# Kernel tuning notes

Hardware: AMD Instinct MI355X
Metric: run time of the kernel (lower is better)

Reference implementation:

```python
import jax, jax.numpy as jnp
import numpy as np

EPS = 1e-6      # vector-neuron epsilon
BN_EPS = 1e-5   # torch BatchNorm eps
NEG = 0.2       # LeakyReLU negative slope
K = 20


def knn_idx(flat, k):
    # flat: [B, D, N] flattened (C*3) features; returns kNN indices [B, N, k]
    xx = jnp.sum(flat * flat, axis=1)                     # [B, N]
    inner = jnp.einsum('bdn,bdm->bnm', flat, flat)        # [B, N, N]
    neg_dist = 2.0 * inner - xx[:, :, None] - xx[:, None, :]
    return jax.lax.top_k(neg_dist, k)[1]                  # [B, N, k]


def graph_feature(x, k):
    # x: [B, C, 3, N] -> [B, 2C, 3, N, k] = cat(neighbor - center, center)
    B, C, _, N = x.shape
    idx = knn_idx(x.reshape(B, C * 3, N), k)              # [B, N, k]
    xt = jnp.transpose(x, (0, 3, 1, 2))                   # [B, N, C, 3]
    nbr = jax.vmap(lambda f, i: f[i])(xt, idx)            # [B, N, k, C, 3]
    ctr = jnp.broadcast_to(xt[:, :, None], nbr.shape)
    feat = jnp.concatenate([nbr - ctr, ctr], axis=3)      # [B, N, k, 2C, 3]
    return jnp.transpose(feat, (0, 3, 4, 1, 2))


def vn_bn(x, w, b):
    # VNBatchNorm (training-mode batch stats): normalize the per-vector norm.
    # x: [B, C, 3, ...]
    norm = jnp.sqrt(jnp.sum(x * x, axis=2)) + EPS         # [B, C, ...]
    axes = (0,) + tuple(range(2, norm.ndim))
    mean = jnp.mean(norm, axis=axes, keepdims=True)
    var = jnp.mean((norm - mean) ** 2, axis=axes, keepdims=True)
    shp = (1, -1) + (1,) * (norm.ndim - 2)
    nbn = (norm - mean) / jnp.sqrt(var + BN_EPS) * w.reshape(shp) + b.reshape(shp)
    return x * jnp.expand_dims(nbn / norm, 2)


def vn_lrelu(x, wf, wd, bnw, bnb):
    # VNLinearLeakyReLU: linear over channel dim, VN batchnorm, directional LeakyReLU
    p = jnp.einsum('oi,bi...->bo...', wf, x)
    p = vn_bn(p, bnw, bnb)
    d = jnp.einsum('oi,bi...->bo...', wd, x)
    dot = jnp.sum(p * d, axis=2, keepdims=True)
    dsq = jnp.sum(d * d, axis=2, keepdims=True)
    mask = (dot >= 0).astype(x.dtype)
    return NEG * p + (1.0 - NEG) * (mask * p + (1.0 - mask) * (p - (dot / (dsq + EPS)) * d))


def setup_inputs() -> dict:
    key = jax.random.key(0)
    ks = jax.random.split(key, 12)
    H, C = 64, 128
    lin = lambda k, o, i: jax.random.normal(k, (o, i), jnp.float32) / np.sqrt(i)
    return {
        'x': jax.random.normal(ks[0], (8, 1024, 3), jnp.float32),
        'w1f': lin(ks[1], H, 2), 'w1d': lin(ks[2], H, 2),
        'bn1w': jnp.ones(H), 'bn1b': jnp.zeros(H),
        'w2f': lin(ks[3], H, 2 * H), 'w2d': lin(ks[4], H, 2 * H),
        'bn2w': jnp.ones(H), 'bn2b': jnp.zeros(H),
        'w3f': lin(ks[5], H, 2 * H), 'w3d': lin(ks[6], H, 2 * H),
        'bn3w': jnp.ones(H), 'bn3b': jnp.zeros(H),
        'w4f': lin(ks[7], H, 2 * H), 'w4d': lin(ks[8], H, 2 * H),
        'bn4w': jnp.ones(H), 'bn4b': jnp.zeros(H),
        'wcf': lin(ks[9], C, 4 * H), 'wcd': lin(ks[10], 1, 4 * H),
        'bncw': jnp.ones(C), 'bncb': jnp.zeros(C),
    }


def reference(x, w1f, w1d, bn1w, bn1b, w2f, w2d, bn2w, bn2b,
              w3f, w3d, bn3w, bn3b, w4f, w4d, bn4w, bn4b,
              wcf, wcd, bncw, bncb):
    pts = jnp.transpose(x, (0, 2, 1))[:, None]            # [B, 1, 3, N]
    h = vn_lrelu(graph_feature(pts, K), w1f, w1d, bn1w, bn1b)
    x1 = jnp.mean(h, axis=-1)                             # [B, H, 3, N]
    h = vn_lrelu(graph_feature(x1, K), w2f, w2d, bn2w, bn2b)
    x2 = jnp.mean(h, axis=-1)
    h = vn_lrelu(graph_feature(x2, K), w3f, w3d, bn3w, bn3b)
    x3 = jnp.mean(h, axis=-1)
    h = vn_lrelu(graph_feature(x3, K), w4f, w4d, bn4w, bn4b)
    x4 = jnp.mean(h, axis=-1)
    cat = jnp.concatenate([x1, x2, x3, x4], axis=1)       # [B, 4H, 3, N]
    out = vn_lrelu(cat, wcf, wcd, bncw, bncb)             # [B, c_dim, 3, N]
    return jnp.mean(out, axis=-1)                         # [B, c_dim, 3]
```

## Files before the change

### kernel.cpp

```cpp
#include <hip/hip_runtime.h>

#define NPTS 1024
#define NB 8
#define KNN 20
#define N3 (3*NPTS)
#define CHT 256
#define BSX (CHT*N3)

constexpr int OFF_X0    = 0;
constexpr int OFF_XFEAT = OFF_X0 + NB*N3;
constexpr int OFF_YAP   = OFF_XFEAT + NB*CHT*N3;
constexpr int OFF_YBP   = OFF_YAP + NB*N3*64;
constexpr int OFF_YAD   = OFF_YBP + NB*N3*64;
constexpr int OFF_YBD   = OFF_YAD + NB*N3*64;
constexpr int OFF_XX    = OFF_YBD + NB*N3*64;
constexpr int OFF_WCFT  = OFF_XX + NB*NPTS;
constexpr int OFF_STATS = OFF_WCFT + 256*128;
constexpr int OFF_IDX   = OFF_STATS + 5*256;
constexpr int OFF_PF    = OFF_YAP;
constexpr int OFF_DF    = OFF_YAD;

__global__ void k_transpose(const float* __restrict__ x, float* __restrict__ x0) {
  int t = blockIdx.x*256 + threadIdx.x;
  int b = t >> 10, n = t & 1023;
  const float* p = x + t*3;
  x0[b*N3 + n]          = p[0];
  x0[b*N3 + NPTS + n]   = p[1];
  x0[b*N3 + 2*NPTS + n] = p[2];
}

__global__ void k_xx(const float* __restrict__ Fb, int bs, int D, float* __restrict__ xx) {
  int t = blockIdx.x*256 + threadIdx.x;
  int b = t >> 10, m = t & 1023;
  const float* f = Fb + b*bs + m;
  float a = 0.f;
  for (int d = 0; d < D; ++d) { float v = f[d*NPTS]; a = fmaf(v, v, a); }
  xx[t] = a;
}

__global__ __launch_bounds__(512) void k_knn2(const float* __restrict__ Fb, int bs, int D,
                                              const float* __restrict__ xx,
                                              int* __restrict__ idxo) {
  __shared__ float xs[8][NPTS];
  int g  = blockIdx.x;
  int wg = (g & 7)*64 + (g >> 3);
  int b  = wg >> 6;
  int n0 = (wg & 63) << 4;
  int tid = threadIdx.x;
  int w = tid >> 6, lane = tid & 63;
  const float* f = Fb + b*bs;

  int row0 = n0 + 2*w, row1 = row0 + 1;
  float acc0[16], acc1[16];
  #pragma unroll
  for (int s = 0; s < 16; ++s) { acc0[s] = 0.f; acc1[s] = 0.f; }

  int nt = (D + 7) >> 3;
  for (int t = 0; t < nt; ++t) {
    int d0 = t << 3;
    int cnt = D - d0; if (cnt > 8) cnt = 8;
    __syncthreads();
    #pragma unroll
    for (int u = 0; u < 4; ++u) {
      int e = tid + (u << 9);
      int dd = e >> 8, mq = (e & 255) << 2;
      if (dd < cnt)
        *(float4*)&xs[dd][mq] = *(const float4*)&f[(d0 + dd)*NPTS + mq];
    }
    __syncthreads();
    for (int dd = 0; dd < cnt; ++dd) {
      float rf0 = xs[dd][row0];
      float rf1 = xs[dd][row1];
      #pragma unroll
      for (int s2 = 0; s2 < 4; ++s2) {
        float4 xm = *(const float4*)&xs[dd][(lane << 2) + (s2 << 8)];
        acc0[s2*4+0] = fmaf(rf0, xm.x, acc0[s2*4+0]);
        acc0[s2*4+1] = fmaf(rf0, xm.y, acc0[s2*4+1]);
        acc0[s2*4+2] = fmaf(rf0, xm.z, acc0[s2*4+2]);
        acc0[s2*4+3] = fmaf(rf0, xm.w, acc0[s2*4+3]);
        acc1[s2*4+0] = fmaf(rf1, xm.x, acc1[s2*4+0]);
        acc1[s2*4+1] = fmaf(rf1, xm.y, acc1[s2*4+1]);
        acc1[s2*4+2] = fmaf(rf1, xm.z, acc1[s2*4+2]);
        acc1[s2*4+3] = fmaf(rf1, xm.w, acc1[s2*4+3]);
      }
    }
  }

  float xxm[16];
  #pragma unroll
  for (int s2 = 0; s2 < 4; ++s2) {
    float4 xv = *(const float4*)&xx[b*NPTS + (lane << 2) + (s2 << 8)];
    xxm[s2*4+0] = xv.x; xxm[s2*4+1] = xv.y; xxm[s2*4+2] = xv.z; xxm[s2*4+3] = xv.w;
  }
  float xxr0 = xx[b*NPTS + row0];
  float xxr1 = xx[b*NPTS + row1];
  #pragma unroll
  for (int s = 0; s < 16; ++s) {
    acc0[s] = (2.f*acc0[s] - xxr0) - xxm[s];
    acc1[s] = (2.f*acc1[s] - xxr1) - xxm[s];
  }

  #pragma unroll
  for (int rr = 0; rr < 2; ++rr) {
    int rown = rr ? row1 : row0;
    unsigned taken = 0u;
    int winm = 0;
    for (int it = 0; it < KNN; ++it) {
      float bv = -3.402823466e38f;
      int   bi = 0x7fffffff;
      int   bsl = 0;
      #pragma unroll
      for (int s = 0; s < 16; ++s) {
        int m = (lane << 2) + ((s >> 2) << 8) + (s & 3);
        float v = rr ? acc1[s] : acc0[s];
        bool ok = (((taken >> s) & 1u) == 0u) && (v > bv);
        bv  = ok ? v : bv;
        bi  = ok ? m : bi;
        bsl = ok ? s : bsl;
      }
      int myi = bi, mysl = bsl;
      #pragma unroll
      for (int off = 1; off < 64; off <<= 1) {
        float ov = __shfl_xor(bv, off, 64);
        int   oi = __shfl_xor(bi, off, 64);
        bool tk = (ov > bv) || (ov == bv && oi < bi);
        bv = tk ? ov : bv;
        bi = tk ? oi : bi;
      }
      if (bi == myi) taken |= (1u << (mysl & 15));
      if (lane == it) winm = bi;
    }
    if (lane < KNN) idxo[(b*NPTS + rown)*KNN + lane] = winm;
  }
}

template<int DIN>
__global__ __launch_bounds__(256) void k_linear3(const float* __restrict__ xin, int bsx,
                                                 const float* __restrict__ w,
                                                 float* __restrict__ yA, float* __restrict__ yB) {
  __shared__ float wA[DIN*64], wB[DIN*64];
  int tid = threadIdx.x;
  for (int e = tid; e < 64*DIN; e += 256) {
    int o = e & 63, i = e >> 6;
    float a = w[o*(2*DIN) + i];
    wA[i*64 + o] = a;
    wB[i*64 + o] = w[o*(2*DIN) + DIN + i] - a;
  }
  __syncthreads();
  int o = tid & 63, ns = tid >> 6;
  int b = blockIdx.y / 3, v = blockIdx.y % 3;
  int n0 = blockIdx.x * 64 + ns * 16;
  const float* xb = xin + b*bsx + v*NPTS + n0;
  float ap[16], bp[16];
  #pragma unroll
  for (int j = 0; j < 16; ++j) { ap[j] = 0.f; bp[j] = 0.f; }
  for (int i = 0; i < DIN; ++i) {
    float wa = wA[i*64 + o], wb = wB[i*64 + o];
    #pragma unroll
    for (int q = 0; q < 4; ++q) {
      float4 xv = *(const float4*)&xb[i*N3 + q*4];
      ap[q*4+0] = fmaf(wa, xv.x, ap[q*4+0]); bp[q*4+0] = fmaf(wb, xv.x, bp[q*4+0]);
      ap[q*4+1] = fmaf(wa, xv.y, ap[q*4+1]); bp[q*4+1] = fmaf(wb, xv.y, bp[q*4+1]);
      ap[q*4+2] = fmaf(wa, xv.z, ap[q*4+2]); bp[q*4+2] = fmaf(wb, xv.z, bp[q*4+2]);
      ap[q*4+3] = fmaf(wa, xv.w, ap[q*4+3]); bp[q*4+3] = fmaf(wb, xv.w, bp[q*4+3]);
    }
  }
  int base = ((b*3 + v)*NPTS + n0)*64 + o;
  #pragma unroll
  for (int j = 0; j < 16; ++j) { yA[base + j*64] = ap[j]; yB[base + j*64] = bp[j]; }
}

__global__ __launch_bounds__(256) void k_stats(const float* __restrict__ yAp, const float* __restrict__ yBp,
                                               const int* __restrict__ idxo, float* __restrict__ statsL) {
  __shared__ float rs[256], rss[256];
  int tid = threadIdx.x; int o = tid & 63, w = tid >> 6;
  int blk = blockIdx.x;
  int b = blk >> 6;
  int n0 = (blk & 63) << 4;
  float s = 0.f, ss = 0.f;
  for (int jj = 0; jj < 4; ++jj) {
    int n = n0 + w + (jj << 2);
    int i0 = (b*3*NPTS + n)*64 + o;
    float c0 = yBp[i0], c1 = yBp[i0 + NPTS*64], c2 = yBp[i0 + 2*NPTS*64];
    const int* ir = idxo + (b*NPTS + n)*KNN;
    for (int kk = 0; kk < KNN; ++kk) {
      int m = ir[kk];
      int g = (b*3*NPTS + m)*64 + o;
      float p0 = yAp[g] + c0;
      float p1 = yAp[g + NPTS*64] + c1;
      float p2 = yAp[g + 2*NPTS*64] + c2;
      float nrm = sqrtf(p0*p0 + p1*p1 + p2*p2) + 1e-6f;
      s += nrm; ss = fmaf(nrm, nrm, ss);
    }
  }
  rs[tid] = s; rss[tid] = ss;
  __syncthreads();
  if (tid < 64) {
    float a  = rs[tid]  + rs[tid+64]  + rs[tid+128]  + rs[tid+192];
    float as = rss[tid] + rss[tid+64] + rss[tid+128] + rss[tid+192];
    atomicAdd(&statsL[tid], a);
    atomicAdd(&statsL[128 + tid], as);
  }
}

__global__ __launch_bounds__(256) void k_apply(const float* __restrict__ yAp, const float* __restrict__ yBp,
                                               const float* __restrict__ yAd, const float* __restrict__ yBd,
                                               const int* __restrict__ idxo, const float* __restrict__ statsL,
                                               const float* __restrict__ bnw, const float* __restrict__ bnb,
                                               float* __restrict__ xfeat, int coff) {
  int tid = threadIdx.x; int o = tid & 63, w = tid >> 6;
  int blk = blockIdx.x;
  int b = blk >> 8;
  int n = ((blk & 255) << 2) + w;
  const float cntInv = 1.f / 163840.f;
  float mean = statsL[o] * cntInv;
  float var  = statsL[128 + o] * cntInv - mean*mean;
  float istd = rsqrtf(var + 1e-5f);
  float wN = bnw[o], bN = bnb[o];
  int i0 = (b*3*NPTS + n)*64 + o;
  float cp0 = yBp[i0], cp1 = yBp[i0 + NPTS*64], cp2 = yBp[i0 + 2*NPTS*64];
  float cd0 = yBd[i0], cd1 = yBd[i0 + NPTS*64], cd2 = yBd[i0 + 2*NPTS*64];
  const int* ir = idxo + (b*NPTS + n)*KNN;
  float a0 = 0.f, a1 = 0.f, a2 = 0.f;
  for (int kk = 0; kk < KNN; ++kk) {
    int m = ir[kk];
    int g = (b*3*NPTS + m)*64 + o;
    float p0 = yAp[g] + cp0, p1 = yAp[g + NPTS*64] + cp1, p2 = yAp[g + 2*NPTS*64] + cp2;
    float d0 = yAd[g] + cd0, d1 = yAd[g + NPTS*64] + cd1, d2 = yAd[g + 2*NPTS*64] + cd2;
    float nrm = sqrtf(p0*p0 + p1*p1 + p2*p2) + 1e-6f;
    float sc = ((nrm - mean)*istd*wN + bN) / nrm;
    p0 *= sc; p1 *= sc; p2 *= sc;
    float dot = p0*d0 + p1*d1 + p2*d2;
    float dsq = d0*d0 + d1*d1 + d2*d2;
    float coef = (dot < 0.f) ? (0.8f * dot / (dsq + 1e-6f)) : 0.f;
    a0 += p0 - coef*d0; a1 += p1 - coef*d1; a2 += p2 - coef*d2;
  }
  int ob = ((b*CHT + coff + o)*3)*NPTS + n;
  xfeat[ob]          = a0 * 0.05f;
  xfeat[ob + NPTS]   = a1 * 0.05f;
  xfeat[ob + 2*NPTS] = a2 * 0.05f;
}

__global__ void k_wcfT(const float* __restrict__ wcf, float* __restrict__ wT) {
  int e = blockIdx.x*256 + threadIdx.x;
  int o = e >> 8, i = e & 255;
  wT[i*128 + o] = wcf[e];
}

__global__ __launch_bounds__(256) void k_pF2(const float* __restrict__ xfeat, const float* __restrict__ wT,
                                             float* __restrict__ pF) {
  __shared__ float xs[256][32];
  int tid = threadIdx.x;
  int b = blockIdx.y / 3, v = blockIdx.y % 3;
  int n0 = blockIdx.x * 32;
  const float* xb = xfeat + b*BSX + v*NPTS + n0;
  #pragma unroll
  for (int u = 0; u < 8; ++u) {
    int e = tid + (u << 8);
    int i = e >> 3, sl = (e & 7) << 2;
    *(float4*)&xs[i][sl] = *(const float4*)&xb[i*N3 + sl];
  }
  __syncthreads();
  int o = tid & 127, h = tid >> 7;
  float a[16];
  #pragma unroll
  for (int j = 0; j < 16; ++j) a[j] = 0.f;
  for (int i = 0; i < 256; ++i) {
    float wv = wT[i*128 + o];
    #pragma unroll
    for (int q = 0; q < 4; ++q) {
      float4 xv = *(const float4*)&xs[i][h*16 + q*4];
      a[q*4+0] = fmaf(wv, xv.x, a[q*4+0]);
      a[q*4+1] = fmaf(wv, xv.y, a[q*4+1]);
      a[q*4+2] = fmaf(wv, xv.z, a[q*4+2]);
      a[q*4+3] = fmaf(wv, xv.w, a[q*4+3]);
    }
  }
  int base = ((b*3 + v)*NPTS + n0 + h*16)*128 + o;
  #pragma unroll
  for (int j = 0; j < 16; ++j) pF[base + j*128] = a[j];
}

__global__ void k_dF(const float* __restrict__ xfeat, const float* __restrict__ wcd,
                     float* __restrict__ dF) {
  int t = blockIdx.x*256 + threadIdx.x;
  int b = t / N3, rem = t % N3;
  const float* xb = xfeat + b*BSX + rem;
  float a = 0.f;
  for (int i = 0; i < 256; ++i) a = fmaf(wcd[i], xb[i*N3], a);
  dF[t] = a;
}

__global__ __launch_bounds__(256) void k_statsF(const float* __restrict__ pF, float* __restrict__ statsF) {
  int tid = threadIdx.x; int o = tid & 127, half = tid >> 7;
  int blk = blockIdx.x;
  int b = blk >> 4, n0 = (blk & 15) << 6;
  float s = 0.f, ss = 0.f;
  for (int j = 0; j < 32; ++j) {
    int n = n0 + half + (j << 1);
    int g = (b*3*NPTS + n)*128 + o;
    float p0 = pF[g], p1 = pF[g + NPTS*128], p2 = pF[g + 2*NPTS*128];
    float nrm = sqrtf(p0*p0 + p1*p1 + p2*p2) + 1e-6f;
    s += nrm; ss = fmaf(nrm, nrm, ss);
  }
  atomicAdd(&statsF[o], s);
  atomicAdd(&statsF[128 + o], ss);
}

__global__ __launch_bounds__(256) void k_final(const float* __restrict__ pF, const float* __restrict__ dF,
                                               const float* __restrict__ statsF,
                                               const float* __restrict__ bncw, const float* __restrict__ bncb,
                                               float* __restrict__ out) {
  int tid = threadIdx.x; int o = tid & 127, half = tid >> 7;
  int blk = blockIdx.x;
  int b = blk >> 3, n0 = (blk & 7) << 7;
  const float cntInv = 1.f / 8192.f;
  float mean = statsF[o] * cntInv;
  float var  = statsF[128 + o] * cntInv - mean*mean;
  float istd = rsqrtf(var + 1e-5f);
  float wN = bncw[o], bN = bncb[o];
  float a0 = 0.f, a1 = 0.f, a2 = 0.f;
  for (int j = 0; j < 64; ++j) {
    int n = n0 + half + (j << 1);
    int g = (b*3*NPTS + n)*128 + o;
    float p0 = pF[g], p1 = pF[g + NPTS*128], p2 = pF[g + 2*NPTS*128];
    int dg = b*N3 + n;
    float d0 = dF[dg], d1 = dF[dg + NPTS], d2 = dF[dg + 2*NPTS];
    float nrm = sqrtf(p0*p0 + p1*p1 + p2*p2) + 1e-6f;
    float sc = ((nrm - mean)*istd*wN + bN) / nrm;
    p0 *= sc; p1 *= sc; p2 *= sc;
    float dot = p0*d0 + p1*d1 + p2*d2;
    float dsq = d0*d0 + d1*d1 + d2*d2;
    float coef = (dot < 0.f) ? (0.8f * dot / (dsq + 1e-6f)) : 0.f;
    a0 += p0 - coef*d0; a1 += p1 - coef*d1; a2 += p2 - coef*d2;
  }
  float scl = 1.f / 1024.f;
  int ob = (b*128 + o)*3;
  atomicAdd(&out[ob],     a0*scl);
  atomicAdd(&out[ob + 1], a1*scl);
  atomicAdd(&out[ob + 2], a2*scl);
}

extern "C" void kernel_launch(void* const* d_in, const int* in_sizes, int n_in,
                              void* d_out, int out_size, void* d_ws, size_t ws_size,
                              hipStream_t stream) {
  (void)in_sizes; (void)n_in; (void)ws_size;
  const float* x = (const float*)d_in[0];
  const float* wF[4]  = {(const float*)d_in[1],  (const float*)d_in[5],
                         (const float*)d_in[9],  (const float*)d_in[13]};
  const float* wD[4]  = {(const float*)d_in[2],  (const float*)d_in[6],
                         (const float*)d_in[10], (const float*)d_in[14]};
  const float* bnW[4] = {(const float*)d_in[3],  (const float*)d_in[7],
                         (const float*)d_in[11], (const float*)d_in[15]};
  const float* bnB[4] = {(const float*)d_in[4],  (const float*)d_in[8],
                         (const float*)d_in[12], (const float*)d_in[16]};
  const float* wcf  = (const float*)d_in[17];
  const float* wcd  = (const float*)d_in[18];
  const float* bncw = (const float*)d_in[19];
  const float* bncb = (const float*)d_in[20];

  float* ws    = (float*)d_ws;
  float* x0    = ws + OFF_X0;
  float* xfeat = ws + OFF_XFEAT;
  float* yAp   = ws + OFF_YAP;
  float* yBp   = ws + OFF_YBP;
  float* yAd   = ws + OFF_YAD;
  float* yBd   = ws + OFF_YBD;
  float* pF    = ws + OFF_PF;
  float* dF    = ws + OFF_DF;
  float* xx    = ws + OFF_XX;
  float* wT    = ws + OFF_WCFT;
  float* stats = ws + OFF_STATS;
  int*   idx   = (int*)(ws + OFF_IDX);

  hipMemsetAsync(stats, 0, 5*256*sizeof(float), stream);
  hipMemsetAsync(d_out, 0, (size_t)out_size*sizeof(float), stream);

  k_transpose<<<NB*NPTS/256, 256, 0, stream>>>(x, x0);
  k_wcfT<<<128, 256, 0, stream>>>(wcf, wT);

  for (int L = 0; L < 4; ++L) {
    const float* fin = (L == 0) ? x0 : (xfeat + (L-1)*64*N3);
    int bs = (L == 0) ? N3 : BSX;
    int D  = (L == 0) ? 3 : 192;
    k_xx<<<NB*NPTS/256, 256, 0, stream>>>(fin, bs, D, xx);
    k_knn2<<<512, 512, 0, stream>>>(fin, bs, D, xx, idx);
    if (L == 0) {
      k_linear3<1><<<dim3(16, 24), 256, 0, stream>>>(fin, bs, wF[0], yAp, yBp);
      k_linear3<1><<<dim3(16, 24), 256, 0, stream>>>(fin, bs, wD[0], yAd, yBd);
    } else {
      k_linear3<64><<<dim3(16, 24), 256, 0, stream>>>(fin, bs, wF[L], yAp, yBp);
      k_linear3<64><<<dim3(16, 24), 256, 0, stream>>>(fin, bs, wD[L], yAd, yBd);
    }
    k_stats<<<512, 256, 0, stream>>>(yAp, yBp, idx, stats + L*256);
    k_apply<<<2048, 256, 0, stream>>>(yAp, yBp, yAd, yBd, idx, stats + L*256,
                                      bnW[L], bnB[L], xfeat, L*64);
  }

  k_pF2<<<dim3(32, 24), 256, 0, stream>>>(xfeat, wT, pF);
  k_dF<<<NB*N3/256, 256, 0, stream>>>(xfeat, wcd, dF);
  k_statsF<<<128, 256, 0, stream>>>(pF, stats + 4*256);
  k_final<<<64, 256, 0, stream>>>(pF, dF, stats + 4*256, bncw, bncb, (float*)d_out);
}
```

Baseline: 1.088 ms.

## Rework kNN selection, widen grids, remap blocks, fuse direction projection into pF

The kNN top-k now encodes scores as order-preserving unsigned keys, packs them with the index into 64-bit keys for a single shuffle reduction, and processes both rows in one loop instead of two sequential passes. k_xx splits the feature dimension across four waves and reduces through shared memory. k_stats, k_statsF and k_final get more, smaller blocks, and k_stats and k_apply use a batch-interleaved block mapping. The wcd direction projection is fused into the pF kernel, reusing the shared-memory tile and dropping one launch plus a full reread of xfeat. The tie-breaking and selection logic changes, and the finer grids issue more atomics.

After: 1.020 ms. -6.3%, faster.

```diff
diff --git a/kernel.cpp b/kernel.cpp
--- a/kernel.cpp
+++ b/kernel.cpp
@@ -29,13 +29,20 @@
   x0[b*N3 + 2*NPTS + n] = p[2];
 }
 
-__global__ void k_xx(const float* __restrict__ Fb, int bs, int D, float* __restrict__ xx) {
-  int t = blockIdx.x*256 + threadIdx.x;
+__global__ __launch_bounds__(256) void k_xx2(const float* __restrict__ Fb, int bs, int D,
+                                             float* __restrict__ xx) {
+  __shared__ float sm[4][64];
+  int tid = threadIdx.x;
+  int p = tid & 63, g = tid >> 6;
+  int t = blockIdx.x * 64 + p;
   int b = t >> 10, m = t & 1023;
+  int s = (D * g) >> 2, e = (D * (g + 1)) >> 2;
   const float* f = Fb + b*bs + m;
   float a = 0.f;
-  for (int d = 0; d < D; ++d) { float v = f[d*NPTS]; a = fmaf(v, v, a); }
-  xx[t] = a;
+  for (int d = s; d < e; ++d) { float v = f[d*NPTS]; a = fmaf(v, v, a); }
+  sm[g][p] = a;
+  __syncthreads();
+  if (g == 0) xx[t] = ((sm[0][p] + sm[1][p]) + sm[2][p]) + sm[3][p];
 }
 
 __global__ __launch_bounds__(512) void k_knn2(const float* __restrict__ Fb, int bs, int D,
@@ -86,51 +93,59 @@
     }
   }
 
-  float xxm[16];
+  unsigned ord0[16], ord1[16];
+  float xxr0 = xx[b*NPTS + row0];
+  float xxr1 = xx[b*NPTS + row1];
   #pragma unroll
   for (int s2 = 0; s2 < 4; ++s2) {
     float4 xv = *(const float4*)&xx[b*NPTS + (lane << 2) + (s2 << 8)];
-    xxm[s2*4+0] = xv.x; xxm[s2*4+1] = xv.y; xxm[s2*4+2] = xv.z; xxm[s2*4+3] = xv.w;
-  }
-  float xxr0 = xx[b*NPTS + row0];
-  float xxr1 = xx[b*NPTS + row1];
-  #pragma unroll
-  for (int s = 0; s < 16; ++s) {
-    acc0[s] = (2.f*acc0[s] - xxr0) - xxm[s];
-    acc1[s] = (2.f*acc1[s] - xxr1) - xxm[s];
-  }
-
-  #pragma unroll
-  for (int rr = 0; rr < 2; ++rr) {
-    int rown = rr ? row1 : row0;
-    unsigned taken = 0u;
-    int winm = 0;
-    for (int it = 0; it < KNN; ++it) {
-      float bv = -3.402823466e38f;
-      int   bi = 0x7fffffff;
-      int   bsl = 0;
-      #pragma unroll
-      for (int s = 0; s < 16; ++s) {
-        int m = (lane << 2) + ((s >> 2) << 8) + (s & 3);
-        float v = rr ? acc1[s] : acc0[s];
-        bool ok = (((taken >> s) & 1u) == 0u) && (v > bv);
-        bv  = ok ? v : bv;
-        bi  = ok ? m : bi;
-        bsl = ok ? s : bsl;
-      }
-      int myi = bi, mysl = bsl;
-      #pragma unroll
-      for (int off = 1; off < 64; off <<= 1) {
-        float ov = __shfl_xor(bv, off, 64);
-        int   oi = __shfl_xor(bi, off, 64);
-        bool tk = (ov > bv) || (ov == bv && oi < bi);
-        bv = tk ? ov : bv;
-        bi = tk ? oi : bi;
-      }
-      if (bi == myi) taken |= (1u << (mysl & 15));
-      if (lane == it) winm = bi;
-    }
-    if (lane < KNN) idxo[(b*NPTS + rown)*KNN + lane] = winm;
+    float xm4[4] = {xv.x, xv.y, xv.z, xv.w};
+    #pragma unroll
+    for (int q = 0; q < 4; ++q) {
+      int s = s2*4 + q;
+      float v0 = (2.f*acc0[s] - xxr0) - xm4[q];
+      float v1 = (2.f*acc1[s] - xxr1) - xm4[q];
+      unsigned u0 = __float_as_uint(v0);
+      unsigned u1 = __float_as_uint(v1);
+      ord0[s] = (u0 & 0x80000000u) ? ~u0 : (u0 | 0x80000000u);
+      ord1[s] = (u1 & 0x80000000u) ? ~u1 : (u1 | 0x80000000u);
+    }
+  }
+
+  unsigned base4L = (unsigned)(lane << 2);
+  unsigned cl0 = 0xFFFFFFFFu, cl1 = 0xFFFFFFFFu;
+  int winm0 = 0, winm1 = 0;
+  for (int it = 0; it < KNN; ++it) {
+    unsigned bo0 = 0u, bc0 = 0u, bo1 = 0u, bc1 = 0u;
+    #pragma unroll
+    for (int s = 0; s < 16; ++s) {
+      const unsigned Cs = (unsigned)(((s >> 2) << 8) | (s & 3));
+      unsigned v0 = ord0[s]; v0 = (cl0 == Cs) ? 0u : v0; ord0[s] = v0;
+      if (v0 > bo0) { bo0 = v0; bc0 = Cs; }
+      unsigned v1 = ord1[s]; v1 = (cl1 == Cs) ? 0u : v1; ord1[s] = v1;
+      if (v1 > bo1) { bo1 = v1; bc1 = Cs; }
+    }
+    unsigned m0 = base4L + bc0, m1 = base4L + bc1;
+    unsigned long long K0 = ((unsigned long long)bo0 << 32) | (unsigned long long)(1023u - m0);
+    unsigned long long K1 = ((unsigned long long)bo1 << 32) | (unsigned long long)(1023u - m1);
+    unsigned long long myK0 = K0, myK1 = K1;
+    #pragma unroll
+    for (int off = 1; off < 64; off <<= 1) {
+      unsigned long long o0 = __shfl_xor(K0, off, 64);
+      unsigned long long o1 = __shfl_xor(K1, off, 64);
+      K0 = (o0 > K0) ? o0 : K0;
+      K1 = (o1 > K1) ? o1 : K1;
+    }
+    cl0 = (K0 == myK0) ? bc0 : 0xFFFFFFFFu;
+    cl1 = (K1 == myK1) ? bc1 : 0xFFFFFFFFu;
+    if (lane == it) {
+      winm0 = 1023 - (int)(unsigned)(K0 & 0xFFFFFFFFull);
+      winm1 = 1023 - (int)(unsigned)(K1 & 0xFFFFFFFFull);
+    }
+  }
+  if (lane < KNN) {
+    idxo[(b*NPTS + row0)*KNN + lane] = winm0;
+    idxo[(b*NPTS + row1)*KNN + lane] = winm1;
   }
 }
 
@@ -170,28 +185,26 @@
   for (int j = 0; j < 16; ++j) { yA[base + j*64] = ap[j]; yB[base + j*64] = bp[j]; }
 }
 
-__global__ __launch_bounds__(256) void k_stats(const float* __restrict__ yAp, const float* __restrict__ yBp,
-                                               const int* __restrict__ idxo, float* __restrict__ statsL) {
+__global__ __launch_bounds__(256) void k_stats2(const float* __restrict__ yAp, const float* __restrict__ yBp,
+                                                const int* __restrict__ idxo, float* __restrict__ statsL) {
   __shared__ float rs[256], rss[256];
   int tid = threadIdx.x; int o = tid & 63, w = tid >> 6;
   int blk = blockIdx.x;
-  int b = blk >> 6;
-  int n0 = (blk & 63) << 4;
+  int wg = ((blk & 7) << 8) | (blk >> 3);
+  int b = wg >> 8;
+  int n = ((wg & 255) << 2) + w;
   float s = 0.f, ss = 0.f;
-  for (int jj = 0; jj < 4; ++jj) {
-    int n = n0 + w + (jj << 2);
-    int i0 = (b*3*NPTS + n)*64 + o;
-    float c0 = yBp[i0], c1 = yBp[i0 + NPTS*64], c2 = yBp[i0 + 2*NPTS*64];
-    const int* ir = idxo + (b*NPTS + n)*KNN;
-    for (int kk = 0; kk < KNN; ++kk) {
-      int m = ir[kk];
-      int g = (b*3*NPTS + m)*64 + o;
-      float p0 = yAp[g] + c0;
-      float p1 = yAp[g + NPTS*64] + c1;
-      float p2 = yAp[g + 2*NPTS*64] + c2;
-      float nrm = sqrtf(p0*p0 + p1*p1 + p2*p2) + 1e-6f;
-      s += nrm; ss = fmaf(nrm, nrm, ss);
-    }
+  int i0 = (b*3*NPTS + n)*64 + o;
+  float c0 = yBp[i0], c1 = yBp[i0 + NPTS*64], c2 = yBp[i0 + 2*NPTS*64];
+  const int* ir = idxo + (b*NPTS + n)*KNN;
+  for (int kk = 0; kk < KNN; ++kk) {
+    int m = ir[kk];
+    int gg = (b*3*NPTS + m)*64 + o;
+    float p0 = yAp[gg] + c0;
+    float p1 = yAp[gg + NPTS*64] + c1;
+    float p2 = yAp[gg + 2*NPTS*64] + c2;
+    float nrm = sqrtf(p0*p0 + p1*p1 + p2*p2) + 1e-6f;
+    s += nrm; ss = fmaf(nrm, nrm, ss);
   }
   rs[tid] = s; rss[tid] = ss;
   __syncthreads();
@@ -210,8 +223,9 @@
                                                float* __restrict__ xfeat, int coff) {
   int tid = threadIdx.x; int o = tid & 63, w = tid >> 6;
   int blk = blockIdx.x;
-  int b = blk >> 8;
-  int n = ((blk & 255) << 2) + w;
+  int wg = ((blk & 7) << 8) | (blk >> 3);
+  int b = wg >> 8;
+  int n = ((wg & 255) << 2) + w;
   const float cntInv = 1.f / 163840.f;
   float mean = statsL[o] * cntInv;
   float var  = statsL[128 + o] * cntInv - mean*mean;
@@ -224,9 +238,9 @@
   float a0 = 0.f, a1 = 0.f, a2 = 0.f;
   for (int kk = 0; kk < KNN; ++kk) {
     int m = ir[kk];
-    int g = (b*3*NPTS + m)*64 + o;
-    float p0 = yAp[g] + cp0, p1 = yAp[g + NPTS*64] + cp1, p2 = yAp[g + 2*NPTS*64] + cp2;
-    float d0 = yAd[g] + cd0, d1 = yAd[g + NPTS*64] + cd1, d2 = yAd[g + 2*NPTS*64] + cd2;
+    int gg = (b*3*NPTS + m)*64 + o;
+    float p0 = yAp[gg] + cp0, p1 = yAp[gg + NPTS*64] + cp1, p2 = yAp[gg + 2*NPTS*64] + cp2;
+    float d0 = yAd[gg] + cd0, d1 = yAd[gg + NPTS*64] + cd1, d2 = yAd[gg + 2*NPTS*64] + cd2;
     float nrm = sqrtf(p0*p0 + p1*p1 + p2*p2) + 1e-6f;
     float sc = ((nrm - mean)*istd*wN + bN) / nrm;
     p0 *= sc; p1 *= sc; p2 *= sc;
@@ -247,9 +261,11 @@
   wT[i*128 + o] = wcf[e];
 }
 
-__global__ __launch_bounds__(256) void k_pF2(const float* __restrict__ xfeat, const float* __restrict__ wT,
-                                             float* __restrict__ pF) {
+__global__ __launch_bounds__(256) void k_pF3(const float* __restrict__ xfeat, const float* __restrict__ wT,
+                                             const float* __restrict__ wcd,
+                                             float* __restrict__ pF, float* __restrict__ dF) {
   __shared__ float xs[256][32];
+  __shared__ float dpart[8][32];
   int tid = threadIdx.x;
   int b = blockIdx.y / 3, v = blockIdx.y % 3;
   int n0 = blockIdx.x * 32;
@@ -279,24 +295,25 @@
   int base = ((b*3 + v)*NPTS + n0 + h*16)*128 + o;
   #pragma unroll
   for (int j = 0; j < 16; ++j) pF[base + j*128] = a[j];
-}
-
-__global__ void k_dF(const float* __restrict__ xfeat, const float* __restrict__ wcd,
-                     float* __restrict__ dF) {
-  int t = blockIdx.x*256 + threadIdx.x;
-  int b = t / N3, rem = t % N3;
-  const float* xb = xfeat + b*BSX + rem;
-  float a = 0.f;
-  for (int i = 0; i < 256; ++i) a = fmaf(wcd[i], xb[i*N3], a);
-  dF[t] = a;
-}
-
-__global__ __launch_bounds__(256) void k_statsF(const float* __restrict__ pF, float* __restrict__ statsF) {
+  int nn = tid & 31, gI = tid >> 5;
+  float dp = 0.f;
+  for (int i = gI*32; i < gI*32 + 32; ++i) dp = fmaf(wcd[i], xs[i][nn], dp);
+  dpart[gI][nn] = dp;
+  __syncthreads();
+  if (tid < 32) {
+    float aa = 0.f;
+    #pragma unroll
+    for (int gq = 0; gq < 8; ++gq) aa += dpart[gq][tid];
+    dF[(b*3 + v)*NPTS + n0 + tid] = aa;
+  }
+}
+
+__global__ __launch_bounds__(256) void k_statsF2(const float* __restrict__ pF, float* __restrict__ statsF) {
   int tid = threadIdx.x; int o = tid & 127, half = tid >> 7;
   int blk = blockIdx.x;
-  int b = blk >> 4, n0 = (blk & 15) << 6;
+  int b = blk >> 6, n0 = (blk & 63) << 4;
   float s = 0.f, ss = 0.f;
-  for (int j = 0; j < 32; ++j) {
+  for (int j = 0; j < 8; ++j) {
     int n = n0 + half + (j << 1);
     int g = (b*3*NPTS + n)*128 + o;
     float p0 = pF[g], p1 = pF[g + NPTS*128], p2 = pF[g + 2*NPTS*128];
@@ -307,20 +324,20 @@
   atomicAdd(&statsF[128 + o], ss);
 }
 
-__global__ __launch_bounds__(256) void k_final(const float* __restrict__ pF, const float* __restrict__ dF,
-                                               const float* __restrict__ statsF,
-                                               const float* __restrict__ bncw, const float* __restrict__ bncb,
-                                               float* __restrict__ out) {
+__global__ __launch_bounds__(256) void k_final2(const float* __restrict__ pF, const float* __restrict__ dF,
+                                                const float* __restrict__ statsF,
+                                                const float* __restrict__ bncw, const float* __restrict__ bncb,
+                                                float* __restrict__ out) {
   int tid = threadIdx.x; int o = tid & 127, half = tid >> 7;
   int blk = blockIdx.x;
-  int b = blk >> 3, n0 = (blk & 7) << 7;
+  int b = blk >> 5, n0 = (blk & 31) << 5;
   const float cntInv = 1.f / 8192.f;
   float mean = statsF[o] * cntInv;
   float var  = statsF[128 + o] * cntInv - mean*mean;
   float istd = rsqrtf(var + 1e-5f);
   float wN = bncw[o], bN = bncb[o];
   float a0 = 0.f, a1 = 0.f, a2 = 0.f;
-  for (int j = 0; j < 64; ++j) {
+  for (int j = 0; j < 16; ++j) {
     int n = n0 + half + (j << 1);
     int g = (b*3*NPTS + n)*128 + o;
     float p0 = pF[g], p1 = pF[g + NPTS*128], p2 = pF[g + 2*NPTS*128];
@@ -383,7 +400,7 @@
     const float* fin = (L == 0) ? x0 : (xfeat + (L-1)*64*N3);
     int bs = (L == 0) ? N3 : BSX;
     int D  = (L == 0) ? 3 : 192;
-    k_xx<<<NB*NPTS/256, 256, 0, stream>>>(fin, bs, D, xx);
+    k_xx2<<<NB*NPTS/64, 256, 0, stream>>>(fin, bs, D, xx);
     k_knn2<<<512, 512, 0, stream>>>(fin, bs, D, xx, idx);
     if (L == 0) {
       k_linear3<1><<<dim3(16, 24), 256, 0, stream>>>(fin, bs, wF[0], yAp, yBp);
@@ -392,13 +409,12 @@
       k_linear3<64><<<dim3(16, 24), 256, 0, stream>>>(fin, bs, wF[L], yAp, yBp);
       k_linear3<64><<<dim3(16, 24), 256, 0, stream>>>(fin, bs, wD[L], yAd, yBd);
     }
-    k_stats<<<512, 256, 0, stream>>>(yAp, yBp, idx, stats + L*256);
+    k_stats2<<<2048, 256, 0, stream>>>(yAp, yBp, idx, stats + L*256);
     k_apply<<<2048, 256, 0, stream>>>(yAp, yBp, yAd, yBd, idx, stats + L*256,
                                       bnW[L], bnB[L], xfeat, L*64);
   }
 
-  k_pF2<<<dim3(32, 24), 256, 0, stream>>>(xfeat, wT, pF);
-  k_dF<<<NB*N3/256, 256, 0, stream>>>(xfeat, wcd, dF);
-  k_statsF<<<128, 256, 0, stream>>>(pF, stats + 4*256);
-  k_final<<<64, 256, 0, stream>>>(pF, dF, stats + 4*256, bncw, bncb, (float*)d_out);
-}
+  k_pF3<<<dim3(32, 24), 256, 0, stream>>>(xfeat, wT, wcd, pF, dF);
+  k_statsF2<<<512, 256, 0, stream>>>(pF, stats + 4*256);
+  k_final2<<<256, 256, 0, stream>>>(pF, dF, stats + 4*256, bncw, bncb, (float*)d_out);
+}
```
